# Kernel optimization log

Measured on AMD Instinct MI355X. Metric: run time of the kernel, lower is better.

## Reference

```python
import jax, jax.numpy as jnp
import numpy as np

H = 300      # hidden_dim == GloVe embedding dim (LSTM output is discarded)
MID = 100    # Scorer hidden width
N = 1024     # sentence length


def setup_inputs() -> dict:
    key = jax.random.key(0)
    k1, k2, k3, k4, k5, k6 = jax.random.split(key, 6)
    sentence = jax.random.normal(k1, (N, H), dtype=jnp.float32)
    target_scores = jax.random.randint(k2, (N,), 0, N + 1)
    # nn.Linear(2H, MID) and nn.Linear(MID, 1) params (uniform fan-in init style)
    lim1 = 1.0 / np.sqrt(2 * H)
    W1 = jax.random.uniform(k3, (MID, 2 * H), dtype=jnp.float32, minval=-lim1, maxval=lim1)
    b1 = jax.random.uniform(k4, (MID,), dtype=jnp.float32, minval=-lim1, maxval=lim1)
    lim2 = 1.0 / np.sqrt(MID)
    W2 = jax.random.uniform(k5, (1, MID), dtype=jnp.float32, minval=-lim2, maxval=lim2)
    b2 = jax.random.uniform(k6, (1,), dtype=jnp.float32, minval=-lim2, maxval=lim2)
    return {"sentence": sentence, "target_scores": target_scores,
            "W1": W1, "b1": b1, "W2": W2, "b2": b2}


def reference(sentence, W1, b1, W2, b2, target_scores):
    n = sentence.shape[0]
    # potential_matches = [zeros(H); sentence] -> [n+1, H]
    pm = jnp.concatenate([jnp.zeros((1, H), sentence.dtype), sentence], axis=0)
    # Split the first Linear over the two concatenated halves and broadcast-add:
    # cat(sentence[i], pm[j]) @ W1^T == sentence[i] @ W1[:, :H]^T + pm[j] @ W1[:, H:]^T
    s1 = jnp.einsum('nh,mh->nm', sentence, W1[:, :H])   # [n, MID]
    s2 = jnp.einsum('ph,mh->pm', pm, W1[:, H:])          # [n+1, MID]
    hidden = jax.nn.sigmoid(s1[:, None, :] + s2[None, :, :] + b1)  # [n, n+1, MID]
    scores = jnp.einsum('npm,om->npo', hidden, W2)[..., 0] + b2[0]  # [n, n+1]
    # L1 loss against one-hot indicator of the true head, averaged over all pairs
    indicator = (jnp.arange(n + 1)[None, :] == target_scores[:, None]).astype(scores.dtype)
    loss = jnp.mean(jnp.abs(scores - indicator))
    score_matrix = jax.nn.softmax(scores, axis=1)
    return loss, score_matrix
```

## Files before the change

### kernel.cpp

```cpp
#include <hip/hip_runtime.h>

#define H     300
#define MID   100
#define NN    1024
#define NP1   1025
#define JST   1088

typedef float v2f __attribute__((ext_vector_type(2)));
static __device__ __forceinline__ v2f sp2(float s) { return (v2f){s, s}; }
static __device__ __forceinline__ v2f fma2(v2f a, v2f b, v2f c) {
    return __builtin_elementwise_fma(a, b, c);
}

template <int CTRL>
static __device__ __forceinline__ float row_ror_add(float v) {
    const int s = __builtin_amdgcn_update_dpp(0, __float_as_int(v), CTRL, 0xF, 0xF, true);
    return v + __int_as_float(s);
}
static __device__ __forceinline__ float swz_xor16_add(float v) {
    const int s = __builtin_amdgcn_ds_swizzle(__float_as_int(v), 0x401F);
    return v + __int_as_float(s);
}
static __device__ __forceinline__ float red32(float v) {
    v = swz_xor16_add(v);
    v = row_ror_add<0x128>(v);
    v = row_ror_add<0x124>(v);
    v = row_ror_add<0x122>(v);
    v = row_ror_add<0x121>(v);
    return v;
}

__global__ __launch_bounds__(512) void precompute_kernel(
    const float* __restrict__ sentence,
    const float* __restrict__ W1,
    const float* __restrict__ b1,
    float* __restrict__ s1b,
    float* __restrict__ E4,
    float* __restrict__ out)
{
    const int tid = threadIdx.x;
    const int iA = blockIdx.x * 2, iB = iA + 1;
    const float NL = -1.4426950408889634f;

    if (blockIdx.x == 0) {
        if (tid == 0) out[0] = 0.0f;
        if (tid < MID)
            E4[(long)((tid >> 2) * JST) * 4 + (tid & 3)] = 1.0f;
    }

    const int lane = tid & 63;
    const int wv   = tid >> 6;
    const int sub  = lane >> 5;
    const int hb   = lane & 31;
    const int half = wv & 1;
    const int mb   = (wv >> 1) * 25;

    const float* sA = sentence + (long)iA * H + hb;
    const float* sB = sentence + (long)iB * H + hb;
    float ra[9], rb[9];
    #pragma unroll
    for (int k = 0; k < 9; ++k) { ra[k] = sA[32 * k]; rb[k] = sB[32 * k]; }
    const bool tl = hb < 12;
    const float ra9 = tl ? sA[288] : 0.0f;
    const float rb9 = tl ? sB[288] : 0.0f;
    const int h9 = 288 + (tl ? hb : 0);

    for (int q = 0; q < 13; ++q) {
        const int off = 2 * q + sub;
        const int m   = mb + (off < 25 ? off : 24);
        const float* wrow = W1 + (long)m * (2 * H) + half * H;

        float aA, aB;
        {
            const float w0 = wrow[hb];
            aA = w0 * ra[0];
            aB = w0 * rb[0];
        }
        #pragma unroll
        for (int k = 1; k < 9; ++k) {
            const float w = wrow[hb + 32 * k];
            aA = __builtin_fmaf(w, ra[k], aA);
            aB = __builtin_fmaf(w, rb[k], aB);
        }
        {
            const float w9 = wrow[h9];
            aA = __builtin_fmaf(w9, ra9, aA);
            aB = __builtin_fmaf(w9, rb9, aB);
        }

        aA = red32(aA);
        aB = red32(aB);

        if (hb == 0 && off < 25) {
            if (half == 0) {
                const float bb = b1[m];
                s1b[iA * MID + m] = aA + bb;
                s1b[iB * MID + m] = aB + bb;
            } else {
                float* base = E4 + (long)((m >> 2) * JST) * 4 + (m & 3);
                base[(long)(iA + 1) * 4] = __builtin_amdgcn_exp2f(aA * NL);
                base[(long)(iB + 1) * 4] = __builtin_amdgcn_exp2f(aB * NL);
            }
        }
    }
}

__global__ __launch_bounds__(512, 2) void main_kernel(
    const float* __restrict__ s1b,
    const float* __restrict__ E4,
    const float* __restrict__ W2,
    const float* __restrict__ b2,
    const int*   __restrict__ target,
    float* __restrict__ out)
{
    __shared__ float4 Fq[MID];
    __shared__ float4 w4sh[MID / 4];
    __shared__ float  tmp[4][104];
    __shared__ float  redl[8];
    __shared__ float4 redm[8];
    __shared__ float4 rede[8];
    __shared__ float  sc4sh[4];
    __shared__ float4 bmax, binv;

    const int i0  = blockIdx.x * 4;
    const int tid = threadIdx.x;
    const int lane = tid & 63, wv = tid >> 6;
    const float NL  = -1.4426950408889634f;
    const float L2E =  1.4426950408889634f;
    const v2f one2 = sp2(1.0f);

    if (tid < MID) {
        Fq[tid] = make_float4(
            __builtin_amdgcn_exp2f(s1b[(i0 + 0) * MID + tid] * NL),
            __builtin_amdgcn_exp2f(s1b[(i0 + 1) * MID + tid] * NL),
            __builtin_amdgcn_exp2f(s1b[(i0 + 2) * MID + tid] * NL),
            __builtin_amdgcn_exp2f(s1b[(i0 + 3) * MID + tid] * NL));
    } else if (tid >= 128 && tid < 128 + MID / 4) {
        const int p = tid - 128;
        w4sh[p] = make_float4(W2[4 * p], W2[4 * p + 1], W2[4 * p + 2], W2[4 * p + 3]);
    }
    const float b2v = b2[0];
    __syncthreads();

    #define LDXA(p_) (*(const float4*)(E4 + ((long)(p_) * JST + tid) * 4))
    #define LDXB(p_) (*(const float4*)(E4 + ((long)(p_) * JST + tid + 512) * 4))

    v2f acc01a = sp2(0.f), acc23a = sp2(0.f);
    v2f acc01b = sp2(0.f), acc23b = sp2(0.f);

    #define QCOL(X, accLo, accHi)                                             \
        do {                                                                  \
            const v2f e0 = sp2((X).x), e1 = sp2((X).y);                       \
            const v2f e2 = sp2((X).z), e3 = sp2((X).w);                       \
            {                                                   \
                const v2f A = fma2(e0, (v2f){F0.x, F0.y}, one2);              \
                const v2f B = fma2(e1, (v2f){F1.x, F1.y}, one2);              \
                const v2f C = fma2(e2, (v2f){F2.x, F2.y}, one2);              \
                const v2f D = fma2(e3, (v2f){F3.x, F3.y}, one2);              \
                const v2f AB = A * B, CD = C * D, P = AB * CD;                \
                const v2f R = {__builtin_amdgcn_rcpf(P.x),                    \
                               __builtin_amdgcn_rcpf(P.y)};                   \
                const v2f n1 = fma2(w0, B, w1 * A);                           \
                const v2f n2 = fma2(w2v, D, w3 * C);                          \
                accLo = fma2(fma2(n1, CD, n2 * AB), R, accLo);                \
            }                                                                 \
            {                                                   \
                const v2f A = fma2(e0, (v2f){F0.z, F0.w}, one2);              \
                const v2f B = fma2(e1, (v2f){F1.z, F1.w}, one2);              \
                const v2f C = fma2(e2, (v2f){F2.z, F2.w}, one2);              \
                const v2f D = fma2(e3, (v2f){F3.z, F3.w}, one2);              \
                const v2f AB = A * B, CD = C * D, P = AB * CD;                \
                const v2f R = {__builtin_amdgcn_rcpf(P.x),                    \
                               __builtin_amdgcn_rcpf(P.y)};                   \
                const v2f n1 = fma2(w0, B, w1 * A);                           \
                const v2f n2 = fma2(w2v, D, w3 * C);                          \
                accHi = fma2(fma2(n1, CD, n2 * AB), R, accHi);                \
            }                                                                 \
        } while (0)

    #define QBODY(p_, XA, XB)                                                 \
        do {                                                                  \
            const float4 F0 = Fq[4 * (p_)];                                   \
            const float4 F1 = Fq[4 * (p_) + 1];                               \
            const float4 F2 = Fq[4 * (p_) + 2];                               \
            const float4 F3 = Fq[4 * (p_) + 3];                               \
            const float4 w  = w4sh[p_];                                       \
            const v2f w0 = sp2(w.x), w1 = sp2(w.y);                           \
            const v2f w2v = sp2(w.z), w3 = sp2(w.w);                          \
            QCOL(XA, acc01a, acc23a);                                         \
            QCOL(XB, acc01b, acc23b);                                         \
        } while (0)

    float4 xa0 = LDXA(0), xb0 = LDXB(0);
    float4 xa1 = LDXA(1), xb1 = LDXB(1);
    #pragma unroll 2
    for (int p = 0; p < 23; ++p) {
        const float4 xan = LDXA(p + 2), xbn = LDXB(p + 2);
        QBODY(p, xa0, xb0);
        xa0 = xa1; xa1 = xan;
        xb0 = xb1; xb1 = xbn;
    }
    QBODY(23, xa0, xb0);
    QBODY(24, xa1, xb1);

    const float sc0a = acc01a.x + b2v, sc1a = acc01a.y + b2v;
    const float sc2a = acc23a.x + b2v, sc3a = acc23a.y + b2v;
    const float sc0b = acc01b.x + b2v, sc1b = acc01b.y + b2v;
    const float sc2b = acc23b.x + b2v, sc3b = acc23b.y + b2v;

    if (tid < MID) {
        const float E = E4[((long)(tid >> 2) * JST + 1024) * 4 + (tid & 3)];
        const float4 F = Fq[tid];
        const float wm = W2[tid];
        tmp[0][tid] = wm * __builtin_amdgcn_rcpf(__builtin_fmaf(E, F.x, 1.f));
        tmp[1][tid] = wm * __builtin_amdgcn_rcpf(__builtin_fmaf(E, F.y, 1.f));
        tmp[2][tid] = wm * __builtin_amdgcn_rcpf(__builtin_fmaf(E, F.z, 1.f));
        tmp[3][tid] = wm * __builtin_amdgcn_rcpf(__builtin_fmaf(E, F.w, 1.f));
    }
    __syncthreads();
    if (wv < 4) {
        float v = tmp[wv][lane] + ((lane < MID - 64) ? tmp[wv][lane + 64] : 0.f);
        #pragma unroll
        for (int off = 32; off > 0; off >>= 1) v += __shfl_down(v, off);
        if (lane == 0) sc4sh[wv] = v + b2v;
    }
    __syncthreads();

    const int tg0 = target[i0], tg1 = target[i0 + 1];
    const int tg2 = target[i0 + 2], tg3 = target[i0 + 3];
    const int jb = tid + 512;
    float ls = fabsf(sc0a - ((tid == tg0) ? 1.f : 0.f))
             + fabsf(sc1a - ((tid == tg1) ? 1.f : 0.f))
             + fabsf(sc2a - ((tid == tg2) ? 1.f : 0.f))
             + fabsf(sc3a - ((tid == tg3) ? 1.f : 0.f))
             + fabsf(sc0b - ((jb == tg0) ? 1.f : 0.f))
             + fabsf(sc1b - ((jb == tg1) ? 1.f : 0.f))
             + fabsf(sc2b - ((jb == tg2) ? 1.f : 0.f))
             + fabsf(sc3b - ((jb == tg3) ? 1.f : 0.f));
    float4 mx = make_float4(fmaxf(sc0a, sc0b), fmaxf(sc1a, sc1b),
                            fmaxf(sc2a, sc2b), fmaxf(sc3a, sc3b));
    if (tid == 0) {
        ls += fabsf(sc4sh[0] - ((1024 == tg0) ? 1.f : 0.f))
            + fabsf(sc4sh[1] - ((1024 == tg1) ? 1.f : 0.f))
            + fabsf(sc4sh[2] - ((1024 == tg2) ? 1.f : 0.f))
            + fabsf(sc4sh[3] - ((1024 == tg3) ? 1.f : 0.f));
        mx.x = fmaxf(mx.x, sc4sh[0]);
        mx.y = fmaxf(mx.y, sc4sh[1]);
        mx.z = fmaxf(mx.z, sc4sh[2]);
        mx.w = fmaxf(mx.w, sc4sh[3]);
    }
    #pragma unroll
    for (int off = 32; off > 0; off >>= 1) {
        ls += __shfl_down(ls, off);
        mx.x = fmaxf(mx.x, __shfl_down(mx.x, off));
        mx.y = fmaxf(mx.y, __shfl_down(mx.y, off));
        mx.z = fmaxf(mx.z, __shfl_down(mx.z, off));
        mx.w = fmaxf(mx.w, __shfl_down(mx.w, off));
    }
    if (lane == 0) { redl[wv] = ls; redm[wv] = mx; }
    __syncthreads();
    if (tid == 0) {
        float L = 0.f;
        float4 M = make_float4(-1e30f, -1e30f, -1e30f, -1e30f);
        #pragma unroll
        for (int k = 0; k < 8; ++k) {
            L += redl[k];
            M.x = fmaxf(M.x, redm[k].x);
            M.y = fmaxf(M.y, redm[k].y);
            M.z = fmaxf(M.z, redm[k].z);
            M.w = fmaxf(M.w, redm[k].w);
        }
        atomicAdd(out, L * (1.0f / ((float)NN * (float)NP1)));
        bmax = M;
    }
    __syncthreads();
    const float4 rm = bmax;

    const float e0a = __builtin_amdgcn_exp2f((sc0a - rm.x) * L2E);
    const float e1a = __builtin_amdgcn_exp2f((sc1a - rm.y) * L2E);
    const float e2a = __builtin_amdgcn_exp2f((sc2a - rm.z) * L2E);
    const float e3a = __builtin_amdgcn_exp2f((sc3a - rm.w) * L2E);
    const float e0b = __builtin_amdgcn_exp2f((sc0b - rm.x) * L2E);
    const float e1b = __builtin_amdgcn_exp2f((sc1b - rm.y) * L2E);
    const float e2b = __builtin_amdgcn_exp2f((sc2b - rm.z) * L2E);
    const float e3b = __builtin_amdgcn_exp2f((sc3b - rm.w) * L2E);
    float4 e4v = make_float4(0.f, 0.f, 0.f, 0.f);
    if (tid == 0) {
        e4v.x = __builtin_amdgcn_exp2f((sc4sh[0] - rm.x) * L2E);
        e4v.y = __builtin_amdgcn_exp2f((sc4sh[1] - rm.y) * L2E);
        e4v.z = __builtin_amdgcn_exp2f((sc4sh[2] - rm.z) * L2E);
        e4v.w = __builtin_amdgcn_exp2f((sc4sh[3] - rm.w) * L2E);
    }
    float4 es = make_float4(e0a + e0b + e4v.x, e1a + e1b + e4v.y,
                            e2a + e2b + e4v.z, e3a + e3b + e4v.w);
    #pragma unroll
    for (int off = 32; off > 0; off >>= 1) {
        es.x += __shfl_down(es.x, off);
        es.y += __shfl_down(es.y, off);
        es.z += __shfl_down(es.z, off);
        es.w += __shfl_down(es.w, off);
    }
    if (lane == 0) rede[wv] = es;
    __syncthreads();
    if (tid == 0) {
        float4 S = make_float4(0.f, 0.f, 0.f, 0.f);
        #pragma unroll
        for (int k = 0; k < 8; ++k) {
            S.x += rede[k].x; S.y += rede[k].y;
            S.z += rede[k].z; S.w += rede[k].w;
        }
        binv = make_float4(1.f / S.x, 1.f / S.y, 1.f / S.z, 1.f / S.w);
    }
    __syncthreads();
    const float4 iv = binv;

    float* o0 = out + 1 + (long)(i0 + 0) * NP1;
    float* o1 = out + 1 + (long)(i0 + 1) * NP1;
    float* o2 = out + 1 + (long)(i0 + 2) * NP1;
    float* o3 = out + 1 + (long)(i0 + 3) * NP1;
    o0[tid] = e0a * iv.x;
    o1[tid] = e1a * iv.y;
    o2[tid] = e2a * iv.z;
    o3[tid] = e3a * iv.w;
    o0[jb] = e0b * iv.x;
    o1[jb] = e1b * iv.y;
    o2[jb] = e2b * iv.z;
    o3[jb] = e3b * iv.w;
    if (tid == 0) {
        o0[1024] = e4v.x * iv.x;
        o1[1024] = e4v.y * iv.y;
        o2[1024] = e4v.z * iv.z;
        o3[1024] = e4v.w * iv.w;
    }
    #undef QBODY
    #undef QCOL
    #undef LDXA
    #undef LDXB
}

extern "C" void kernel_launch(void* const* d_in, const int* in_sizes, int n_in,
                              void* d_out, int out_size, void* d_ws, size_t ws_size,
                              hipStream_t stream) {
    const float* sentence = (const float*)d_in[0];
    const int*   target   = (const int*)  d_in[1];
    const float* W1       = (const float*)d_in[2];
    const float* b1       = (const float*)d_in[3];
    const float* W2       = (const float*)d_in[4];
    const float* b2       = (const float*)d_in[5];
    float* out = (float*)d_out;

    float* s1b = (float*)d_ws;
    float* E4  = s1b + NN * MID;

    precompute_kernel<<<NN / 2, 512, 0, stream>>>(sentence, W1, b1, s1b, E4, out);
    main_kernel<<<NN / 4, 512, 0, stream>>>(s1b, E4, W2, b2, target, out);
}
```

Baseline: 91.70 us.

## Fuse precompute and main kernels into one cooperative kernel with grid sync

Merges the W1 projection precompute into the main scoring kernel and launches it cooperatively, with a grid-wide barrier between the projection phase and the pairwise phase. Each block now computes the s1 projections for its own four rows directly into shared memory, which removes the s1b workspace round trip, and writes the s2 exponentials for four rows into E4. This removes one kernel launch and the inter-kernel gap. In exchange it pays for a grid sync, drops the min-blocks-per-CU launch bound hint, and raises register pressure in the precompute phase.

```diff
diff --git a/kernel.cpp b/kernel.cpp
--- a/kernel.cpp
+++ b/kernel.cpp
@@ -1,10 +1,13 @@
 #include <hip/hip_runtime.h>
+#include <hip/hip_cooperative_groups.h>
 
 #define H     300
 #define MID   100
 #define NN    1024
 #define NP1   1025
 #define JST   1088
+
+namespace cg = cooperative_groups;
 
 typedef float v2f __attribute__((ext_vector_type(2)));
 static __device__ __forceinline__ v2f sp2(float s) { return (v2f){s, s}; }
@@ -30,87 +33,14 @@
     return v;
 }
 
-__global__ __launch_bounds__(512) void precompute_kernel(
+__global__ __launch_bounds__(512) void fused_kernel(
     const float* __restrict__ sentence,
     const float* __restrict__ W1,
     const float* __restrict__ b1,
-    float* __restrict__ s1b,
-    float* __restrict__ E4,
-    float* __restrict__ out)
-{
-    const int tid = threadIdx.x;
-    const int iA = blockIdx.x * 2, iB = iA + 1;
-    const float NL = -1.4426950408889634f;
-
-    if (blockIdx.x == 0) {
-        if (tid == 0) out[0] = 0.0f;
-        if (tid < MID)
-            E4[(long)((tid >> 2) * JST) * 4 + (tid & 3)] = 1.0f;
-    }
-
-    const int lane = tid & 63;
-    const int wv   = tid >> 6;
-    const int sub  = lane >> 5;
-    const int hb   = lane & 31;
-    const int half = wv & 1;
-    const int mb   = (wv >> 1) * 25;
-
-    const float* sA = sentence + (long)iA * H + hb;
-    const float* sB = sentence + (long)iB * H + hb;
-    float ra[9], rb[9];
-    #pragma unroll
-    for (int k = 0; k < 9; ++k) { ra[k] = sA[32 * k]; rb[k] = sB[32 * k]; }
-    const bool tl = hb < 12;
-    const float ra9 = tl ? sA[288] : 0.0f;
-    const float rb9 = tl ? sB[288] : 0.0f;
-    const int h9 = 288 + (tl ? hb : 0);
-
-    for (int q = 0; q < 13; ++q) {
-        const int off = 2 * q + sub;
-        const int m   = mb + (off < 25 ? off : 24);
-        const float* wrow = W1 + (long)m * (2 * H) + half * H;
-
-        float aA, aB;
-        {
-            const float w0 = wrow[hb];
-            aA = w0 * ra[0];
-            aB = w0 * rb[0];
-        }
-        #pragma unroll
-        for (int k = 1; k < 9; ++k) {
-            const float w = wrow[hb + 32 * k];
-            aA = __builtin_fmaf(w, ra[k], aA);
-            aB = __builtin_fmaf(w, rb[k], aB);
-        }
-        {
-            const float w9 = wrow[h9];
-            aA = __builtin_fmaf(w9, ra9, aA);
-            aB = __builtin_fmaf(w9, rb9, aB);
-        }
-
-        aA = red32(aA);
-        aB = red32(aB);
-
-        if (hb == 0 && off < 25) {
-            if (half == 0) {
-                const float bb = b1[m];
-                s1b[iA * MID + m] = aA + bb;
-                s1b[iB * MID + m] = aB + bb;
-            } else {
-                float* base = E4 + (long)((m >> 2) * JST) * 4 + (m & 3);
-                base[(long)(iA + 1) * 4] = __builtin_amdgcn_exp2f(aA * NL);
-                base[(long)(iB + 1) * 4] = __builtin_amdgcn_exp2f(aB * NL);
-            }
-        }
-    }
-}
-
-__global__ __launch_bounds__(512, 2) void main_kernel(
-    const float* __restrict__ s1b,
-    const float* __restrict__ E4,
     const float* __restrict__ W2,
     const float* __restrict__ b2,
     const int*   __restrict__ target,
+    float* __restrict__ E4,
     float* __restrict__ out)
 {
     __shared__ float4 Fq[MID];
@@ -122,25 +52,94 @@
     __shared__ float  sc4sh[4];
     __shared__ float4 bmax, binv;
 
+    const int tid = threadIdx.x;
     const int i0  = blockIdx.x * 4;
-    const int tid = threadIdx.x;
-    const int lane = tid & 63, wv = tid >> 6;
     const float NL  = -1.4426950408889634f;
     const float L2E =  1.4426950408889634f;
-    const v2f one2 = sp2(1.0f);
-
-    if (tid < MID) {
-        Fq[tid] = make_float4(
-            __builtin_amdgcn_exp2f(s1b[(i0 + 0) * MID + tid] * NL),
-            __builtin_amdgcn_exp2f(s1b[(i0 + 1) * MID + tid] * NL),
-            __builtin_amdgcn_exp2f(s1b[(i0 + 2) * MID + tid] * NL),
-            __builtin_amdgcn_exp2f(s1b[(i0 + 3) * MID + tid] * NL));
-    } else if (tid >= 128 && tid < 128 + MID / 4) {
+
+    if (blockIdx.x == 0) {
+        if (tid == 0) atomicExch(out, 0.0f);
+        if (tid < MID)
+            E4[(long)((tid >> 2) * JST) * 4 + (tid & 3)] = 1.0f;
+    }
+    if (tid >= 128 && tid < 128 + MID / 4) {
         const int p = tid - 128;
         w4sh[p] = make_float4(W2[4 * p], W2[4 * p + 1], W2[4 * p + 2], W2[4 * p + 3]);
     }
+
+    {
+        const int grp = tid >> 5;
+        const int hb  = tid & 31;
+        const float* sp0 = sentence + (long)(i0 + 0) * H + hb;
+        const float* sp1 = sentence + (long)(i0 + 1) * H + hb;
+        const float* sp2v = sentence + (long)(i0 + 2) * H + hb;
+        const float* sp3 = sentence + (long)(i0 + 3) * H + hb;
+        float r0[10], r1[10], r2[10], r3[10];
+        #pragma unroll
+        for (int k = 0; k < 9; ++k) {
+            r0[k] = sp0[32 * k]; r1[k] = sp1[32 * k];
+            r2[k] = sp2v[32 * k]; r3[k] = sp3[32 * k];
+        }
+        const bool tl = hb < 12;
+        r0[9] = tl ? sp0[288] : 0.f;
+        r1[9] = tl ? sp1[288] : 0.f;
+        r2[9] = tl ? sp2v[288] : 0.f;
+        r3[9] = tl ? sp3[288] : 0.f;
+        const int h9 = 288 + (tl ? hb : 0);
+
+        for (int s = 0; s < 13; ++s) {
+            const int p  = s * 16 + grp;
+            const int pc = p < 200 ? p : 199;
+            const int m  = pc >> 1, half = pc & 1;
+            const float* wrow = W1 + (long)m * (2 * H) + half * H;
+
+            float a0, a1, a2, a3;
+            {
+                const float w = wrow[hb];
+                a0 = w * r0[0]; a1 = w * r1[0]; a2 = w * r2[0]; a3 = w * r3[0];
+            }
+            #pragma unroll
+            for (int k = 1; k < 9; ++k) {
+                const float w = wrow[hb + 32 * k];
+                a0 = __builtin_fmaf(w, r0[k], a0);
+                a1 = __builtin_fmaf(w, r1[k], a1);
+                a2 = __builtin_fmaf(w, r2[k], a2);
+                a3 = __builtin_fmaf(w, r3[k], a3);
+            }
+            {
+                const float w = wrow[h9];
+                a0 = __builtin_fmaf(w, r0[9], a0);
+                a1 = __builtin_fmaf(w, r1[9], a1);
+                a2 = __builtin_fmaf(w, r2[9], a2);
+                a3 = __builtin_fmaf(w, r3[9], a3);
+            }
+
+            a0 = red32(a0); a1 = red32(a1); a2 = red32(a2); a3 = red32(a3);
+
+            if (hb == 0 && p < 200) {
+                if (half == 0) {
+                    const float bb = b1[m];
+                    Fq[m] = make_float4(
+                        __builtin_amdgcn_exp2f((a0 + bb) * NL),
+                        __builtin_amdgcn_exp2f((a1 + bb) * NL),
+                        __builtin_amdgcn_exp2f((a2 + bb) * NL),
+                        __builtin_amdgcn_exp2f((a3 + bb) * NL));
+                } else {
+                    float* base = E4 + (long)((m >> 2) * JST) * 4 + (m & 3);
+                    base[(long)(i0 + 1) * 4] = __builtin_amdgcn_exp2f(a0 * NL);
+                    base[(long)(i0 + 2) * 4] = __builtin_amdgcn_exp2f(a1 * NL);
+                    base[(long)(i0 + 3) * 4] = __builtin_amdgcn_exp2f(a2 * NL);
+                    base[(long)(i0 + 4) * 4] = __builtin_amdgcn_exp2f(a3 * NL);
+                }
+            }
+        }
+    }
+
+    cg::this_grid().sync();
+
+    const int lane = tid & 63, wv = tid >> 6;
+    const v2f one2 = sp2(1.0f);
     const float b2v = b2[0];
-    __syncthreads();
 
     #define LDXA(p_) (*(const float4*)(E4 + ((long)(p_) * JST + tid) * 4))
     #define LDXB(p_) (*(const float4*)(E4 + ((long)(p_) * JST + tid + 512) * 4))
@@ -348,10 +347,12 @@
     const float* W2       = (const float*)d_in[4];
     const float* b2       = (const float*)d_in[5];
     float* out = (float*)d_out;
-
-    float* s1b = (float*)d_ws;
-    float* E4  = s1b + NN * MID;
-
-    precompute_kernel<<<NN / 2, 512, 0, stream>>>(sentence, W1, b1, s1b, E4, out);
-    main_kernel<<<NN / 4, 512, 0, stream>>>(s1b, E4, W2, b2, target, out);
-}
+    float* E4  = (float*)d_ws;
+
+    void* args[] = {
+        (void*)&sentence, (void*)&W1, (void*)&b1, (void*)&W2,
+        (void*)&b2, (void*)&target, (void*)&E4, (void*)&out
+    };
+    hipLaunchCooperativeKernel((const void*)fused_kernel,
+                               dim3(NN / 4), dim3(512), args, 0, stream);
+}
```

New measurement: 128.1 us. 39.7% more time.

## Process two rows per block in main kernel and precompute exp of s1

Applied to the files above, without the earlier changes.

The main kernel now handles two sentence rows per block instead of four, doubling the grid to 512 blocks, and its launch bounds are raised to allow four blocks per CU. The exp of the first-half projection moves into the precompute kernel, so the main kernel loads ready-made factors. This aims for more parallelism and occupancy across the CUs. In exchange, each block reuses each E4 load for fewer rows, so total E4 traffic doubles, and the tighter register budget may cause spills.

```diff
diff --git a/kernel.cpp b/kernel.cpp
--- a/kernel.cpp
+++ b/kernel.cpp
@@ -30,11 +30,11 @@
     return v;
 }
 
-__global__ __launch_bounds__(512) void precompute_kernel(
+__global__ __launch_bounds__(512, 4) void precompute_kernel(
     const float* __restrict__ sentence,
     const float* __restrict__ W1,
     const float* __restrict__ b1,
-    float* __restrict__ s1b,
+    float* __restrict__ Fg,
     float* __restrict__ E4,
     float* __restrict__ out)
 {
@@ -94,8 +94,8 @@
         if (hb == 0 && off < 25) {
             if (half == 0) {
                 const float bb = b1[m];
-                s1b[iA * MID + m] = aA + bb;
-                s1b[iB * MID + m] = aB + bb;
+                Fg[iA * MID + m] = __builtin_amdgcn_exp2f((aA + bb) * NL);
+                Fg[iB * MID + m] = __builtin_amdgcn_exp2f((aB + bb) * NL);
             } else {
                 float* base = E4 + (long)((m >> 2) * JST) * 4 + (m & 3);
                 base[(long)(iA + 1) * 4] = __builtin_amdgcn_exp2f(aA * NL);
@@ -105,36 +105,31 @@
     }
 }
 
-__global__ __launch_bounds__(512, 2) void main_kernel(
-    const float* __restrict__ s1b,
+__global__ __launch_bounds__(512, 4) void main_kernel(
+    const float* __restrict__ Fg,
     const float* __restrict__ E4,
     const float* __restrict__ W2,
     const float* __restrict__ b2,
     const int*   __restrict__ target,
     float* __restrict__ out)
 {
-    __shared__ float4 Fq[MID];
+    __shared__ v2f    Fq2[MID];
     __shared__ float4 w4sh[MID / 4];
-    __shared__ float  tmp[4][104];
+    __shared__ float  tmp[2][104];
     __shared__ float  redl[8];
-    __shared__ float4 redm[8];
-    __shared__ float4 rede[8];
-    __shared__ float  sc4sh[4];
-    __shared__ float4 bmax, binv;
-
-    const int i0  = blockIdx.x * 4;
+    __shared__ v2f    redm[8];
+    __shared__ v2f    rede[8];
+    __shared__ float  sc4sh[2];
+    __shared__ v2f    bmax2, binv2;
+
+    const int i0  = blockIdx.x * 2;
     const int tid = threadIdx.x;
     const int lane = tid & 63, wv = tid >> 6;
-    const float NL  = -1.4426950408889634f;
-    const float L2E =  1.4426950408889634f;
+    const float L2E = 1.4426950408889634f;
     const v2f one2 = sp2(1.0f);
 
     if (tid < MID) {
-        Fq[tid] = make_float4(
-            __builtin_amdgcn_exp2f(s1b[(i0 + 0) * MID + tid] * NL),
-            __builtin_amdgcn_exp2f(s1b[(i0 + 1) * MID + tid] * NL),
-            __builtin_amdgcn_exp2f(s1b[(i0 + 2) * MID + tid] * NL),
-            __builtin_amdgcn_exp2f(s1b[(i0 + 3) * MID + tid] * NL));
+        Fq2[tid] = (v2f){Fg[(i0 + 0) * MID + tid], Fg[(i0 + 1) * MID + tid]};
     } else if (tid >= 128 && tid < 128 + MID / 4) {
         const int p = tid - 128;
         w4sh[p] = make_float4(W2[4 * p], W2[4 * p + 1], W2[4 * p + 2], W2[4 * p + 3]);
@@ -145,50 +140,34 @@
     #define LDXA(p_) (*(const float4*)(E4 + ((long)(p_) * JST + tid) * 4))
     #define LDXB(p_) (*(const float4*)(E4 + ((long)(p_) * JST + tid + 512) * 4))
 
-    v2f acc01a = sp2(0.f), acc23a = sp2(0.f);
-    v2f acc01b = sp2(0.f), acc23b = sp2(0.f);
-
-    #define QCOL(X, accLo, accHi)                                             \
+    v2f acca = sp2(0.f);
+    v2f accb = sp2(0.f);
+
+    #define QCOL(X, acc)                                                      \
         do {                                                                  \
-            const v2f e0 = sp2((X).x), e1 = sp2((X).y);                       \
-            const v2f e2 = sp2((X).z), e3 = sp2((X).w);                       \
-            {                                                   \
-                const v2f A = fma2(e0, (v2f){F0.x, F0.y}, one2);              \
-                const v2f B = fma2(e1, (v2f){F1.x, F1.y}, one2);              \
-                const v2f C = fma2(e2, (v2f){F2.x, F2.y}, one2);              \
-                const v2f D = fma2(e3, (v2f){F3.x, F3.y}, one2);              \
-                const v2f AB = A * B, CD = C * D, P = AB * CD;                \
-                const v2f R = {__builtin_amdgcn_rcpf(P.x),                    \
-                               __builtin_amdgcn_rcpf(P.y)};                   \
-                const v2f n1 = fma2(w0, B, w1 * A);                           \
-                const v2f n2 = fma2(w2v, D, w3 * C);                          \
-                accLo = fma2(fma2(n1, CD, n2 * AB), R, accLo);                \
-            }                                                                 \
-            {                                                   \
-                const v2f A = fma2(e0, (v2f){F0.z, F0.w}, one2);              \
-                const v2f B = fma2(e1, (v2f){F1.z, F1.w}, one2);              \
-                const v2f C = fma2(e2, (v2f){F2.z, F2.w}, one2);              \
-                const v2f D = fma2(e3, (v2f){F3.z, F3.w}, one2);              \
-                const v2f AB = A * B, CD = C * D, P = AB * CD;                \
-                const v2f R = {__builtin_amdgcn_rcpf(P.x),                    \
-                               __builtin_amdgcn_rcpf(P.y)};                   \
-                const v2f n1 = fma2(w0, B, w1 * A);                           \
-                const v2f n2 = fma2(w2v, D, w3 * C);                          \
-                accHi = fma2(fma2(n1, CD, n2 * AB), R, accHi);                \
-            }                                                                 \
+            const v2f A = fma2(sp2((X).x), F0, one2);                         \
+            const v2f B = fma2(sp2((X).y), F1, one2);                         \
+            const v2f C = fma2(sp2((X).z), F2, one2);                         \
+            const v2f D = fma2(sp2((X).w), F3, one2);                         \
+            const v2f AB = A * B, CD = C * D, P = AB * CD;                    \
+            const v2f R = {__builtin_amdgcn_rcpf(P.x),                        \
+                           __builtin_amdgcn_rcpf(P.y)};                       \
+            const v2f n1 = fma2(w0, B, w1 * A);                               \
+            const v2f n2 = fma2(w2v, D, w3 * C);                              \
+            acc = fma2(fma2(n1, CD, n2 * AB), R, acc);                        \
         } while (0)
 
     #define QBODY(p_, XA, XB)                                                 \
         do {                                                                  \
-            const float4 F0 = Fq[4 * (p_)];                                   \
-            const float4 F1 = Fq[4 * (p_) + 1];                               \
-            const float4 F2 = Fq[4 * (p_) + 2];                               \
-            const float4 F3 = Fq[4 * (p_) + 3];                               \
-            const float4 w  = w4sh[p_];                                       \
+            const v2f F0 = Fq2[4 * (p_)];                                     \
+            const v2f F1 = Fq2[4 * (p_) + 1];                                 \
+            const v2f F2 = Fq2[4 * (p_) + 2];                                 \
+            const v2f F3 = Fq2[4 * (p_) + 3];                                 \
+            const float4 w = w4sh[p_];                                        \
             const v2f w0 = sp2(w.x), w1 = sp2(w.y);                           \
             const v2f w2v = sp2(w.z), w3 = sp2(w.w);                          \
-            QCOL(XA, acc01a, acc23a);                                         \
-            QCOL(XB, acc01b, acc23b);                                         \
+            QCOL(XA, acca);                                                   \
+            QCOL(XB, accb);                                                   \
         } while (0)
 
     float4 xa0 = LDXA(0), xb0 = LDXB(0);
@@ -203,22 +182,18 @@
     QBODY(23, xa0, xb0);
     QBODY(24, xa1, xb1);
 
-    const float sc0a = acc01a.x + b2v, sc1a = acc01a.y + b2v;
-    const float sc2a = acc23a.x + b2v, sc3a = acc23a.y + b2v;
-    const float sc0b = acc01b.x + b2v, sc1b = acc01b.y + b2v;
-    const float sc2b = acc23b.x + b2v, sc3b = acc23b.y + b2v;
+    const float sc0a = acca.x + b2v, sc1a = acca.y + b2v;
+    const float sc0b = accb.x + b2v, sc1b = accb.y + b2v;
 
     if (tid < MID) {
         const float E = E4[((long)(tid >> 2) * JST + 1024) * 4 + (tid & 3)];
-        const float4 F = Fq[tid];
+        const v2f F = Fq2[tid];
         const float wm = W2[tid];
         tmp[0][tid] = wm * __builtin_amdgcn_rcpf(__builtin_fmaf(E, F.x, 1.f));
         tmp[1][tid] = wm * __builtin_amdgcn_rcpf(__builtin_fmaf(E, F.y, 1.f));
-        tmp[2][tid] = wm * __builtin_amdgcn_rcpf(__builtin_fmaf(E, F.z, 1.f));
-        tmp[3][tid] = wm * __builtin_amdgcn_rcpf(__builtin_fmaf(E, F.w, 1.f));
-    }
-    __syncthreads();
-    if (wv < 4) {
+    }
+    __syncthreads();
+    if (wv < 2) {
         float v = tmp[wv][lane] + ((lane < MID - 64) ? tmp[wv][lane + 64] : 0.f);
         #pragma unroll
         for (int off = 32; off > 0; off >>= 1) v += __shfl_down(v, off);
@@ -227,110 +202,76 @@
     __syncthreads();
 
     const int tg0 = target[i0], tg1 = target[i0 + 1];
-    const int tg2 = target[i0 + 2], tg3 = target[i0 + 3];
     const int jb = tid + 512;
     float ls = fabsf(sc0a - ((tid == tg0) ? 1.f : 0.f))
              + fabsf(sc1a - ((tid == tg1) ? 1.f : 0.f))
-             + fabsf(sc2a - ((tid == tg2) ? 1.f : 0.f))
-             + fabsf(sc3a - ((tid == tg3) ? 1.f : 0.f))
              + fabsf(sc0b - ((jb == tg0) ? 1.f : 0.f))
-             + fabsf(sc1b - ((jb == tg1) ? 1.f : 0.f))
-             + fabsf(sc2b - ((jb == tg2) ? 1.f : 0.f))
-             + fabsf(sc3b - ((jb == tg3) ? 1.f : 0.f));
-    float4 mx = make_float4(fmaxf(sc0a, sc0b), fmaxf(sc1a, sc1b),
-                            fmaxf(sc2a, sc2b), fmaxf(sc3a, sc3b));
+             + fabsf(sc1b - ((jb == tg1) ? 1.f : 0.f));
+    v2f mx = {fmaxf(sc0a, sc0b), fmaxf(sc1a, sc1b)};
     if (tid == 0) {
         ls += fabsf(sc4sh[0] - ((1024 == tg0) ? 1.f : 0.f))
-            + fabsf(sc4sh[1] - ((1024 == tg1) ? 1.f : 0.f))
-            + fabsf(sc4sh[2] - ((1024 == tg2) ? 1.f : 0.f))
-            + fabsf(sc4sh[3] - ((1024 == tg3) ? 1.f : 0.f));
+            + fabsf(sc4sh[1] - ((1024 == tg1) ? 1.f : 0.f));
         mx.x = fmaxf(mx.x, sc4sh[0]);
         mx.y = fmaxf(mx.y, sc4sh[1]);
-        mx.z = fmaxf(mx.z, sc4sh[2]);
-        mx.w = fmaxf(mx.w, sc4sh[3]);
     }
     #pragma unroll
     for (int off = 32; off > 0; off >>= 1) {
         ls += __shfl_down(ls, off);
         mx.x = fmaxf(mx.x, __shfl_down(mx.x, off));
         mx.y = fmaxf(mx.y, __shfl_down(mx.y, off));
-        mx.z = fmaxf(mx.z, __shfl_down(mx.z, off));
-        mx.w = fmaxf(mx.w, __shfl_down(mx.w, off));
     }
     if (lane == 0) { redl[wv] = ls; redm[wv] = mx; }
     __syncthreads();
     if (tid == 0) {
         float L = 0.f;
-        float4 M = make_float4(-1e30f, -1e30f, -1e30f, -1e30f);
+        v2f M = {-1e30f, -1e30f};
         #pragma unroll
         for (int k = 0; k < 8; ++k) {
             L += redl[k];
             M.x = fmaxf(M.x, redm[k].x);
             M.y = fmaxf(M.y, redm[k].y);
-            M.z = fmaxf(M.z, redm[k].z);
-            M.w = fmaxf(M.w, redm[k].w);
         }
         atomicAdd(out, L * (1.0f / ((float)NN * (float)NP1)));
-        bmax = M;
-    }
-    __syncthreads();
-    const float4 rm = bmax;
+        bmax2 = M;
+    }
+    __syncthreads();
+    const v2f rm = bmax2;
 
     const float e0a = __builtin_amdgcn_exp2f((sc0a - rm.x) * L2E);
     const float e1a = __builtin_amdgcn_exp2f((sc1a - rm.y) * L2E);
-    const float e2a = __builtin_amdgcn_exp2f((sc2a - rm.z) * L2E);
-    const float e3a = __builtin_amdgcn_exp2f((sc3a - rm.w) * L2E);
     const float e0b = __builtin_amdgcn_exp2f((sc0b - rm.x) * L2E);
     const float e1b = __builtin_amdgcn_exp2f((sc1b - rm.y) * L2E);
-    const float e2b = __builtin_amdgcn_exp2f((sc2b - rm.z) * L2E);
-    const float e3b = __builtin_amdgcn_exp2f((sc3b - rm.w) * L2E);
-    float4 e4v = make_float4(0.f, 0.f, 0.f, 0.f);
+    v2f e4v = sp2(0.f);
     if (tid == 0) {
         e4v.x = __builtin_amdgcn_exp2f((sc4sh[0] - rm.x) * L2E);
         e4v.y = __builtin_amdgcn_exp2f((sc4sh[1] - rm.y) * L2E);
-        e4v.z = __builtin_amdgcn_exp2f((sc4sh[2] - rm.z) * L2E);
-        e4v.w = __builtin_amdgcn_exp2f((sc4sh[3] - rm.w) * L2E);
-    }
-    float4 es = make_float4(e0a + e0b + e4v.x, e1a + e1b + e4v.y,
-                            e2a + e2b + e4v.z, e3a + e3b + e4v.w);
+    }
+    v2f es = {e0a + e0b + e4v.x, e1a + e1b + e4v.y};
     #pragma unroll
     for (int off = 32; off > 0; off >>= 1) {
         es.x += __shfl_down(es.x, off);
         es.y += __shfl_down(es.y, off);
-        es.z += __shfl_down(es.z, off);
-        es.w += __shfl_down(es.w, off);
     }
     if (lane == 0) rede[wv] = es;
     __syncthreads();
     if (tid == 0) {
-        float4 S = make_float4(0.f, 0.f, 0.f, 0.f);
-        #pragma unroll
-        for (int k = 0; k < 8; ++k) {
-            S.x += rede[k].x; S.y += rede[k].y;
-            S.z += rede[k].z; S.w += rede[k].w;
-        }
-        binv = make_float4(1.f / S.x, 1.f / S.y, 1.f / S.z, 1.f / S.w);
-    }
-    __syncthreads();
-    const float4 iv = binv;
+        v2f S = sp2(0.f);
+        #pragma unroll
+        for (int k = 0; k < 8; ++k) { S.x += rede[k].x; S.y += rede[k].y; }
+        binv2 = (v2f){1.f / S.x, 1.f / S.y};
+    }
+    __syncthreads();
+    const v2f iv = binv2;
 
     float* o0 = out + 1 + (long)(i0 + 0) * NP1;
     float* o1 = out + 1 + (long)(i0 + 1) * NP1;
-    float* o2 = out + 1 + (long)(i0 + 2) * NP1;
-    float* o3 = out + 1 + (long)(i0 + 3) * NP1;
     o0[tid] = e0a * iv.x;
     o1[tid] = e1a * iv.y;
-    o2[tid] = e2a * iv.z;
-    o3[tid] = e3a * iv.w;
     o0[jb] = e0b * iv.x;
     o1[jb] = e1b * iv.y;
-    o2[jb] = e2b * iv.z;
-    o3[jb] = e3b * iv.w;
     if (tid == 0) {
         o0[1024] = e4v.x * iv.x;
         o1[1024] = e4v.y * iv.y;
-        o2[1024] = e4v.z * iv.z;
-        o3[1024] = e4v.w * iv.w;
     }
     #undef QBODY
     #undef QCOL
@@ -349,9 +290,9 @@
     const float* b2       = (const float*)d_in[5];
     float* out = (float*)d_out;
 
-    float* s1b = (float*)d_ws;
-    float* E4  = s1b + NN * MID;
-
-    precompute_kernel<<<NN / 2, 512, 0, stream>>>(sentence, W1, b1, s1b, E4, out);
-    main_kernel<<<NN / 4, 512, 0, stream>>>(s1b, E4, W2, b2, target, out);
-}
+    float* Fg = (float*)d_ws;
+    float* E4 = Fg + NN * MID;
+
+    precompute_kernel<<<NN / 2, 512, 0, stream>>>(sentence, W1, b1, Fg, E4, out);
+    main_kernel<<<NN / 2, 512, 0, stream>>>(Fg, E4, W2, b2, target, out);
+}
```

Result: no change. 92.32 us (+0.7%).
